# Kernel optimization log

Hardware: AMD Instinct MI355X
Metric: run time of the kernel (lower is better)

Reference implementation:

```python
import jax, jax.numpy as jnp
import numpy as np


def setup_inputs() -> dict:
    key = jax.random.key(0)
    ks = jax.random.split(key, 5)
    N, D, H, E = 8192, 1024, 4096, 8
    s = 0.02
    return {
        "x": jax.random.normal(ks[0], (N, D), jnp.float32),
        "Wr": jax.random.normal(ks[1], (D, E), jnp.float32) * s,
        "br": jnp.zeros((E,), jnp.float32),
        "W1": jax.random.normal(ks[2], (E, D, H), jnp.float32) * s,
        "b1": jnp.zeros((E, H), jnp.float32),
        "W2": jax.random.normal(ks[3], (E, H, D), jnp.float32) * s,
        "b2": jnp.zeros((E, D), jnp.float32),
        "k": 2,
    }


def reference(x, Wr, br, W1, b1, W2, b2, k):
    # Router (eval mode: no gate noise)
    logits = x @ Wr + br                      # [N, E]
    scores = jax.nn.softmax(logits, axis=-1)  # [N, E]
    topk_vals, topk_inds = jax.lax.top_k(scores, k)  # [N, k]
    N, E = scores.shape
    # dispatch_mask: zeros scattered with top-k probabilities
    dispatch_mask = jnp.zeros_like(scores).at[
        jnp.arange(N)[:, None], topk_inds
    ].set(topk_vals)                          # [N, E]
    # Dense all-expert FFN compute (faithful to the original wasteful pattern)
    h = jax.nn.relu(jnp.einsum('nd,edh->neh', x, W1) + b1)   # [N, E, H]
    expert_outputs = jnp.einsum('neh,ehd->ned', h, W2) + b2  # [N, E, D]
    output = jnp.einsum('ned,ne->nd', expert_outputs, dispatch_mask)  # [N, D]
    # Load-balancing aux loss (torch.var is unbiased, ddof=1)
    importance = dispatch_mask.sum(axis=0)    # [E]
    imp_mean = jnp.mean(importance)
    imp_var = jnp.var(importance, ddof=1)
    aux_loss = imp_var / (imp_mean ** 2 + 1e-9)
    return output, aux_loss
```

## Files before the change

### kernel.cpp

```cpp
#include <hip/hip_runtime.h>
#include <hip/hip_bf16.h>


#define NTOK 8192
#define DDIM 1024
#define HDIM 4096
#define NEXP 8
#define NASSIGN (NTOK * 2)
#define MAX_MT 72
#define KSPLIT 4

typedef __bf16 bf16_t;
typedef __bf16 bf16x4 __attribute__((ext_vector_type(4)));
typedef __bf16 bf16x8 __attribute__((ext_vector_type(8)));
typedef float f32x4 __attribute__((ext_vector_type(4)));

#define GLOAD16(gptr, lptr)                                                    \
  __builtin_amdgcn_global_load_lds(                                            \
      (const __attribute__((address_space(1))) void*)(gptr),                   \
      (__attribute__((address_space(3))) void*)(lptr), 16, 0, 0)


__global__ void __launch_bounds__(256) transpose_cvt_kernel(
    const float* __restrict__ in, bf16_t* __restrict__ out, int R, int C) {
  __shared__ float tile[32][33];
  const size_t mat = (size_t)R * C;
  const float* ip = in + (size_t)blockIdx.z * mat;
  bf16_t* op = out + (size_t)blockIdx.z * mat;
  const int c0 = blockIdx.x * 32, r0 = blockIdx.y * 32;
  const int tx = threadIdx.x, ty = threadIdx.y;
#pragma unroll
  for (int i = 0; i < 4; ++i) {
    const int r = ty + 8 * i;
    tile[r][tx] = ip[(size_t)(r0 + r) * C + (c0 + tx)];
  }
  __syncthreads();
#pragma unroll
  for (int i = 0; i < 4; ++i) {
    const int r = ty + 8 * i;
    op[(size_t)(c0 + r) * R + (r0 + tx)] = (bf16_t)tile[tx][r];
  }
}


__global__ void __launch_bounds__(256) router_kernel(
    const float* __restrict__ x, const float* __restrict__ Wr,
    const float* __restrict__ br, int2* __restrict__ ids,
    float2* __restrict__ prs, int* __restrict__ counts,
    bf16_t* __restrict__ xb) {
  const int n = blockIdx.x;
  const int t = threadIdx.x;
  const float4 xv = ((const float4*)(x + (size_t)n * DDIM))[t];
  bf16x4 o;
  o[0] = (bf16_t)xv.x; o[1] = (bf16_t)xv.y;
  o[2] = (bf16_t)xv.z; o[3] = (bf16_t)xv.w;
  ((bf16x4*)(xb + (size_t)n * DDIM))[t] = o;

  float acc[NEXP];
#pragma unroll
  for (int e = 0; e < NEXP; ++e) acc[e] = 0.f;
  const float xq[4] = {xv.x, xv.y, xv.z, xv.w};
#pragma unroll
  for (int q = 0; q < 4; ++q) {
    const float* w = Wr + (size_t)(4 * t + q) * NEXP;
#pragma unroll
    for (int e = 0; e < NEXP; ++e) acc[e] += xq[q] * w[e];
  }
  __shared__ float red[256][NEXP];
#pragma unroll
  for (int e = 0; e < NEXP; ++e) red[t][e] = acc[e];
  __syncthreads();
  for (int s = 128; s >= 1; s >>= 1) {
    if (t < s) {
#pragma unroll
      for (int e = 0; e < NEXP; ++e) red[t][e] += red[t + s][e];
    }
    __syncthreads();
  }
  if (t == 0) {
    float l[NEXP];
#pragma unroll
    for (int e = 0; e < NEXP; ++e) l[e] = red[0][e] + br[e];
    int i1 = 0; float v1 = l[0];
    for (int e = 1; e < NEXP; ++e)
      if (l[e] > v1) { v1 = l[e]; i1 = e; }
    int i2 = (i1 == 0) ? 1 : 0; float v2 = l[i2];
    for (int e = 0; e < NEXP; ++e)
      if (e != i1 && l[e] > v2) { v2 = l[e]; i2 = e; }
    float denom = 0.f;
    for (int e = 0; e < NEXP; ++e) denom += expf(l[e] - v1);
    const float p1 = 1.f / denom;
    const float p2 = expf(v2 - v1) / denom;
    ids[n] = make_int2(i1, i2);
    prs[n] = make_float2(p1, p2);
    atomicAdd(&counts[i1], 1);
    atomicAdd(&counts[i2], 1);
  }
}

__global__ void __launch_bounds__(256) scan_aux_kernel(
    const int* __restrict__ counts, int* __restrict__ offsets,
    int* __restrict__ tmap, const int2* __restrict__ ids,
    const float2* __restrict__ prs, float* __restrict__ aux_out) {
  const int t = threadIdx.x;
  if (t == 0) {
    int off = 0, nt = 0;
    for (int e = 0; e < NEXP; ++e) {
      offsets[e] = off;
      const int c = counts[e];
      for (int m0 = 0; m0 < c; m0 += 256) {
        tmap[nt] = e;
        tmap[MAX_MT + nt] = m0;
        ++nt;
      }
      off += c;
    }
    offsets[NEXP] = off;
    tmap[2 * MAX_MT] = nt;
  }
  float imp[NEXP];
#pragma unroll
  for (int e = 0; e < NEXP; ++e) imp[e] = 0.f;
  for (int n = t; n < NTOK; n += 256) {
    const int2 id = ids[n];
    const float2 pr = prs[n];
#pragma unroll
    for (int e = 0; e < NEXP; ++e)
      imp[e] += (id.x == e ? pr.x : 0.f) + (id.y == e ? pr.y : 0.f);
  }
  __shared__ float red[256][NEXP];
#pragma unroll
  for (int e = 0; e < NEXP; ++e) red[t][e] = imp[e];
  __syncthreads();
  for (int s = 128; s >= 1; s >>= 1) {
    if (t < s) {
#pragma unroll
      for (int e = 0; e < NEXP; ++e) red[t][e] += red[t + s][e];
    }
    __syncthreads();
  }
  if (t == 0) {
    float m = 0.f;
    for (int e = 0; e < NEXP; ++e) m += red[0][e];
    m *= (1.f / NEXP);
    float v = 0.f;
    for (int e = 0; e < NEXP; ++e) {
      const float d = red[0][e] - m;
      v += d * d;
    }
    v *= (1.f / (NEXP - 1));
    aux_out[0] = v / (m * m + 1e-9f);
  }
}

__global__ void __launch_bounds__(256) scatter_kernel(
    const int2* __restrict__ ids, const float2* __restrict__ prs,
    const int* __restrict__ offsets, int* __restrict__ cursor,
    int* __restrict__ btok, float* __restrict__ bprob) {
  const int n = blockIdx.x * 256 + threadIdx.x;
  if (n >= NTOK) return;
  const int2 id = ids[n];
  const float2 pr = prs[n];
  int p = atomicAdd(&cursor[id.x], 1);
  btok[offsets[id.x] + p] = n;
  bprob[offsets[id.x] + p] = pr.x;
  p = atomicAdd(&cursor[id.y], 1);
  btok[offsets[id.y] + p] = n;
  bprob[offsets[id.y] + p] = pr.y;
}


__global__ void __launch_bounds__(512, 2) gemm1_kernel(
    const bf16_t* __restrict__ xb, const bf16_t* __restrict__ W1t,
    const float* __restrict__ b1, const int* __restrict__ btok,
    const int* __restrict__ offsets, const int* __restrict__ counts,
    const int* __restrict__ tmap, bf16_t* __restrict__ h) {
  const int tidx = blockIdx.y;
  if (tidx >= tmap[2 * MAX_MT]) return;
  const int e = tmap[tidx];
  const int m0 = tmap[MAX_MT + tidx];
  const int cnt = counts[e];
  const int aoff = offsets[e];
  const int n0 = blockIdx.x * 256;

  __shared__ __align__(16) bf16_t Al[2][256 * 64];
  __shared__ __align__(16) bf16_t Bl[2][256 * 64];

  const int tid = threadIdx.x;
  const int wave = tid >> 6;
  const int lane = tid & 63;

  const bf16_t* asrc[4];
  const bf16_t* bsrc[4];
#pragma unroll
  for (int j = 0; j < 4; ++j) {
    const int c = j * 512 + tid;
    const int r = c >> 3;
    const int kc = (c & 7) * 8;
    int arow = m0 + r;
    if (arow > cnt - 1) arow = cnt - 1;
    asrc[j] = xb + (size_t)btok[aoff + arow] * DDIM + kc;
    bsrc[j] = W1t + ((size_t)e * HDIM + n0 + r) * DDIM + kc;
  }

  f32x4 acc[8][4];
#pragma unroll
  for (int mf = 0; mf < 8; ++mf)
#pragma unroll
    for (int nf = 0; nf < 4; ++nf) acc[mf][nf] = (f32x4){0.f, 0.f, 0.f, 0.f};

  const int wr = (wave >> 2) * 128;
  const int wc = (wave & 3) * 64;
  const int lrow = lane & 15;
  const int lk8 = (lane >> 4) * 8;

  auto stage = [&](int b, int t) {
    const int ko = t * 64;
    char* Ab = (char*)&Al[b][0] + wave * 1024;
    char* Bb = (char*)&Bl[b][0] + wave * 1024;
#pragma unroll
    for (int j = 0; j < 4; ++j) {
      GLOAD16(asrc[j] + ko, Ab + j * 8192);
      GLOAD16(bsrc[j] + ko, Bb + j * 8192);
    }
  };
  auto compute = [&](int b) {
    const bf16_t* Ab = &Al[b][0];
    const bf16_t* Bb = &Bl[b][0];
    __builtin_amdgcn_s_setprio(1);
#pragma unroll
    for (int ks = 0; ks < 2; ++ks) {
      bf16x8 af[8], bfr[4];
#pragma unroll
      for (int mf = 0; mf < 8; ++mf)
        af[mf] = *(const bf16x8*)&Ab[(wr + mf * 16 + lrow) * 64 + ks * 32 + lk8];
#pragma unroll
      for (int nf = 0; nf < 4; ++nf)
        bfr[nf] = *(const bf16x8*)&Bb[(wc + nf * 16 + lrow) * 64 + ks * 32 + lk8];
#pragma unroll
      for (int mf = 0; mf < 8; ++mf)
#pragma unroll
        for (int nf = 0; nf < 4; ++nf)
          acc[mf][nf] = __builtin_amdgcn_mfma_f32_16x16x32_bf16(
              af[mf], bfr[nf], acc[mf][nf], 0, 0, 0);
    }
    __builtin_amdgcn_s_setprio(0);
  };

  stage(0, 0);
  __syncthreads();
#pragma unroll
  for (int t = 0; t < 16; t += 2) {
    stage(1, t + 1);
    compute(0);
    __syncthreads();
    if (t + 2 < 16) stage(0, t + 2);
    compute(1);
    __syncthreads();
  }

  const int rbase = (lane >> 4) * 4;
  const float* b1e = b1 + (size_t)e * HDIM + n0;
#pragma unroll
  for (int nf = 0; nf < 4; ++nf) {
    const int cl = wc + nf * 16 + lrow;
    const float bb = b1e[cl];
#pragma unroll
    for (int mf = 0; mf < 8; ++mf) {
#pragma unroll
      for (int r = 0; r < 4; ++r) {
        const int grow = wr + mf * 16 + rbase + r;
        if (m0 + grow < cnt)
          h[(size_t)(aoff + m0 + grow) * HDIM + (n0 + cl)] =
              (bf16_t)fmaxf(acc[mf][nf][r] + bb, 0.f);
      }
    }
  }
}

__global__ void __launch_bounds__(512, 2) gemm2_kernel(
    const bf16_t* __restrict__ h, const bf16_t* __restrict__ W2t,
    const float* __restrict__ b2, const int* __restrict__ btok,
    const float* __restrict__ bprob, const int* __restrict__ offsets,
    const int* __restrict__ counts, const int* __restrict__ tmap,
    float* __restrict__ out) {
  const int tidx = blockIdx.y >> 2;
  const int kch = blockIdx.y & 3;
  if (tidx >= tmap[2 * MAX_MT]) return;
  const int e = tmap[tidx];
  const int m0 = tmap[MAX_MT + tidx];
  const int cnt = counts[e];
  const int aoff = offsets[e];
  const int n0 = blockIdx.x * 256;

  __shared__ __align__(16) bf16_t Al[2][256 * 64];
  __shared__ __align__(16) bf16_t Bl[2][256 * 64];

  const int tid = threadIdx.x;
  const int wave = tid >> 6;
  const int lane = tid & 63;

  const bf16_t* asrc[4];
  const bf16_t* bsrc[4];
#pragma unroll
  for (int j = 0; j < 4; ++j) {
    const int c = j * 512 + tid;
    const int r = c >> 3;
    const int kc = (c & 7) * 8 + kch * 1024;
    int arow = m0 + r;
    if (arow > cnt - 1) arow = cnt - 1;
    asrc[j] = h + (size_t)(aoff + arow) * HDIM + kc;
    bsrc[j] = W2t + ((size_t)e * DDIM + n0 + r) * HDIM + kc;
  }

  f32x4 acc[8][4];
#pragma unroll
  for (int mf = 0; mf < 8; ++mf)
#pragma unroll
    for (int nf = 0; nf < 4; ++nf) acc[mf][nf] = (f32x4){0.f, 0.f, 0.f, 0.f};

  const int wr = (wave >> 2) * 128;
  const int wc = (wave & 3) * 64;
  const int lrow = lane & 15;
  const int lk8 = (lane >> 4) * 8;

  auto stage = [&](int b, int t) {
    const int ko = t * 64;
    char* Ab = (char*)&Al[b][0] + wave * 1024;
    char* Bb = (char*)&Bl[b][0] + wave * 1024;
#pragma unroll
    for (int j = 0; j < 4; ++j) {
      GLOAD16(asrc[j] + ko, Ab + j * 8192);
      GLOAD16(bsrc[j] + ko, Bb + j * 8192);
    }
  };
  auto compute = [&](int b) {
    const bf16_t* Ab = &Al[b][0];
    const bf16_t* Bb = &Bl[b][0];
    __builtin_amdgcn_s_setprio(1);
#pragma unroll
    for (int ks = 0; ks < 2; ++ks) {
      bf16x8 af[8], bfr[4];
#pragma unroll
      for (int mf = 0; mf < 8; ++mf)
        af[mf] = *(const bf16x8*)&Ab[(wr + mf * 16 + lrow) * 64 + ks * 32 + lk8];
#pragma unroll
      for (int nf = 0; nf < 4; ++nf)
        bfr[nf] = *(const bf16x8*)&Bb[(wc + nf * 16 + lrow) * 64 + ks * 32 + lk8];
#pragma unroll
      for (int mf = 0; mf < 8; ++mf)
#pragma unroll
        for (int nf = 0; nf < 4; ++nf)
          acc[mf][nf] = __builtin_amdgcn_mfma_f32_16x16x32_bf16(
              af[mf], bfr[nf], acc[mf][nf], 0, 0, 0);
    }
    __builtin_amdgcn_s_setprio(0);
  };

  stage(0, 0);
  __syncthreads();
#pragma unroll
  for (int t = 0; t < 16; t += 2) {
    stage(1, t + 1);
    compute(0);
    __syncthreads();
    if (t + 2 < 16) stage(0, t + 2);
    compute(1);
    __syncthreads();
  }

  const int rbase = (lane >> 4) * 4;
  const float* b2e = b2 + (size_t)e * DDIM + n0;
  float bb[4];
#pragma unroll
  for (int nf = 0; nf < 4; ++nf)
    bb[nf] = (kch == 0) ? b2e[wc + nf * 16 + lrow] : 0.f;
#pragma unroll
  for (int mf = 0; mf < 8; ++mf) {
#pragma unroll
    for (int r = 0; r < 4; ++r) {
      const int grow = wr + mf * 16 + rbase + r;
      if (m0 + grow < cnt) {
        const int assign = aoff + m0 + grow;
        const int tok = btok[assign];
        const float p = bprob[assign];
        float* orow = out + (size_t)tok * DDIM + n0;
#pragma unroll
        for (int nf = 0; nf < 4; ++nf) {
          const int cl = wc + nf * 16 + lrow;
          atomicAdd(&orow[cl], (acc[mf][nf][r] + bb[nf]) * p);
        }
      }
    }
  }
}


extern "C" void kernel_launch(void* const* d_in, const int* in_sizes, int n_in,
                              void* d_out, int out_size, void* d_ws,
                              size_t ws_size, hipStream_t stream) {
  const float* x = (const float*)d_in[0];
  const float* Wr = (const float*)d_in[1];
  const float* br = (const float*)d_in[2];
  const float* W1 = (const float*)d_in[3];
  const float* b1 = (const float*)d_in[4];
  const float* W2 = (const float*)d_in[5];
  const float* b2 = (const float*)d_in[6];

  char* w = (char*)d_ws;
  auto alloc = [&](size_t bytes) -> char* {
    char* p = w;
    w += (bytes + 255) & ~(size_t)255;
    return p;
  };
  bf16_t* xb = (bf16_t*)alloc((size_t)NTOK * DDIM * 2);
  bf16_t* W1t = (bf16_t*)alloc((size_t)NEXP * DDIM * HDIM * 2);
  bf16_t* W2t = (bf16_t*)alloc((size_t)NEXP * DDIM * HDIM * 2);
  bf16_t* hbuf = (bf16_t*)alloc((size_t)NASSIGN * HDIM * 2);
  int* btok = (int*)alloc(NASSIGN * 4);
  float* bprob = (float*)alloc(NASSIGN * 4);
  int2* ids = (int2*)alloc(NTOK * 8);
  float2* prs = (float2*)alloc(NTOK * 8);
  int* ctrl = (int*)alloc(64);
  int* offsets = (int*)alloc(64);
  int* tmap = (int*)alloc((2 * MAX_MT + 1) * 4);
  int* counts = ctrl;
  int* cursor = ctrl + 8;
  (void)in_sizes; (void)n_in; (void)ws_size;

  float* out = (float*)d_out;

  hipMemsetAsync(d_out, 0, (size_t)out_size * 4, stream);
  hipMemsetAsync(ctrl, 0, 64, stream);

  transpose_cvt_kernel<<<dim3(HDIM / 32, DDIM / 32, NEXP), dim3(32, 8), 0,
                         stream>>>(W1, W1t, DDIM, HDIM);
  transpose_cvt_kernel<<<dim3(DDIM / 32, HDIM / 32, NEXP), dim3(32, 8), 0,
                         stream>>>(W2, W2t, HDIM, DDIM);
  router_kernel<<<NTOK, 256, 0, stream>>>(x, Wr, br, ids, prs, counts, xb);
  scan_aux_kernel<<<1, 256, 0, stream>>>(counts, offsets, tmap, ids, prs,
                                         out + (size_t)NTOK * DDIM);
  scatter_kernel<<<NTOK / 256, 256, 0, stream>>>(ids, prs, offsets, cursor,
                                                 btok, bprob);
  gemm1_kernel<<<dim3(HDIM / 256, MAX_MT, 1), 512, 0, stream>>>(
      xb, W1t, b1, btok, offsets, counts, tmap, hbuf);
  gemm2_kernel<<<dim3(DDIM / 256, MAX_MT * KSPLIT, 1), 512, 0, stream>>>(
      hbuf, W2t, b2, btok, bprob, offsets, counts, tmap, out);
}
```

Baseline: 1.015 ms.

## Retile expert GEMMs to 128x128 triple-buffered, swizzled LDS with XCD remap

Both grouped GEMMs move from 256x256 tiles with 512 threads and double buffering to 128x128x32 tiles with 256 threads, triple-buffered global_load_lds staging, explicit vmcnt waits and raw barriers. LDS slots are XOR-swizzled to avoid bank conflicts, and blocks are remapped across XCDs for cache locality. The router reduction now uses wave shuffles, and the weight transpose writes packed bf16 pairs from 64-row tiles. Smaller tiles give more blocks and better occupancy, at the cost of lower per-block operand reuse and more atomic epilogue traffic.

After: 941.3 us. 7.2% less time.

```diff
diff --git a/kernel.cpp b/kernel.cpp
--- a/kernel.cpp
+++ b/kernel.cpp
@@ -7,10 +7,12 @@
 #define HDIM 4096
 #define NEXP 8
 #define NASSIGN (NTOK * 2)
-#define MAX_MT 72
-#define KSPLIT 4
+#define MAX_MT 135
+#define GRID1 (32 * MAX_MT)
+#define GRID2 (8 * 4 * MAX_MT)
 
 typedef __bf16 bf16_t;
+typedef __bf16 bf16x2 __attribute__((ext_vector_type(2)));
 typedef __bf16 bf16x4 __attribute__((ext_vector_type(4)));
 typedef __bf16 bf16x8 __attribute__((ext_vector_type(8)));
 typedef float f32x4 __attribute__((ext_vector_type(4)));
@@ -20,28 +22,36 @@
       (const __attribute__((address_space(1))) void*)(gptr),                   \
       (__attribute__((address_space(3))) void*)(lptr), 16, 0, 0)
 
+#define VMCNT(n) asm volatile("s_waitcnt vmcnt(" #n ")" ::: "memory")
+
+__device__ __forceinline__ int xcd_swz(int orig, int nwg) {
+  const int cpx = nwg >> 3;
+  return (orig & 7) * cpx + (orig >> 3);
+}
 
 __global__ void __launch_bounds__(256) transpose_cvt_kernel(
     const float* __restrict__ in, bf16_t* __restrict__ out, int R, int C) {
-  __shared__ float tile[32][33];
+  __shared__ float tile[64][33];
   const size_t mat = (size_t)R * C;
   const float* ip = in + (size_t)blockIdx.z * mat;
   bf16_t* op = out + (size_t)blockIdx.z * mat;
-  const int c0 = blockIdx.x * 32, r0 = blockIdx.y * 32;
+  const int c0 = blockIdx.x * 32, r0 = blockIdx.y * 64;
   const int tx = threadIdx.x, ty = threadIdx.y;
 #pragma unroll
-  for (int i = 0; i < 4; ++i) {
+  for (int i = 0; i < 8; ++i) {
     const int r = ty + 8 * i;
     tile[r][tx] = ip[(size_t)(r0 + r) * C + (c0 + tx)];
   }
   __syncthreads();
 #pragma unroll
-  for (int i = 0; i < 4; ++i) {
-    const int r = ty + 8 * i;
-    op[(size_t)(c0 + r) * R + (r0 + tx)] = (bf16_t)tile[tx][r];
-  }
-}
-
+  for (int j = 0; j < 4; ++j) {
+    const int c = ty + 8 * j;
+    bf16x2 v;
+    v[0] = (bf16_t)tile[2 * tx][c];
+    v[1] = (bf16_t)tile[2 * tx + 1][c];
+    *(bf16x2*)(op + (size_t)(c0 + c) * R + r0 + 2 * tx) = v;
+  }
+}
 
 __global__ void __launch_bounds__(256) router_kernel(
     const float* __restrict__ x, const float* __restrict__ Wr,
@@ -50,6 +60,7 @@
     bf16_t* __restrict__ xb) {
   const int n = blockIdx.x;
   const int t = threadIdx.x;
+  const int wave = t >> 6, lane = t & 63;
   const float4 xv = ((const float4*)(x + (size_t)n * DDIM))[t];
   bf16x4 o;
   o[0] = (bf16_t)xv.x; o[1] = (bf16_t)xv.y;
@@ -66,21 +77,20 @@
 #pragma unroll
     for (int e = 0; e < NEXP; ++e) acc[e] += xq[q] * w[e];
   }
-  __shared__ float red[256][NEXP];
-#pragma unroll
-  for (int e = 0; e < NEXP; ++e) red[t][e] = acc[e];
+#pragma unroll
+  for (int off = 32; off >= 1; off >>= 1)
+#pragma unroll
+    for (int e = 0; e < NEXP; ++e) acc[e] += __shfl_down(acc[e], off);
+  __shared__ float red[4][NEXP];
+  if (lane == 0)
+#pragma unroll
+    for (int e = 0; e < NEXP; ++e) red[wave][e] = acc[e];
   __syncthreads();
-  for (int s = 128; s >= 1; s >>= 1) {
-    if (t < s) {
-#pragma unroll
-      for (int e = 0; e < NEXP; ++e) red[t][e] += red[t + s][e];
-    }
-    __syncthreads();
-  }
   if (t == 0) {
     float l[NEXP];
 #pragma unroll
-    for (int e = 0; e < NEXP; ++e) l[e] = red[0][e] + br[e];
+    for (int e = 0; e < NEXP; ++e)
+      l[e] = ((red[0][e] + red[1][e]) + (red[2][e] + red[3][e])) + br[e];
     int i1 = 0; float v1 = l[0];
     for (int e = 1; e < NEXP; ++e)
       if (l[e] > v1) { v1 = l[e]; i1 = e; }
@@ -89,10 +99,8 @@
       if (e != i1 && l[e] > v2) { v2 = l[e]; i2 = e; }
     float denom = 0.f;
     for (int e = 0; e < NEXP; ++e) denom += expf(l[e] - v1);
-    const float p1 = 1.f / denom;
-    const float p2 = expf(v2 - v1) / denom;
     ids[n] = make_int2(i1, i2);
-    prs[n] = make_float2(p1, p2);
+    prs[n] = make_float2(1.f / denom, expf(v2 - v1) / denom);
     atomicAdd(&counts[i1], 1);
     atomicAdd(&counts[i2], 1);
   }
@@ -108,7 +116,7 @@
     for (int e = 0; e < NEXP; ++e) {
       offsets[e] = off;
       const int c = counts[e];
-      for (int m0 = 0; m0 < c; m0 += 256) {
+      for (int m0 = 0; m0 < c; m0 += 128) {
         tmap[nt] = e;
         tmap[MAX_MT + nt] = m0;
         ++nt;
@@ -170,94 +178,106 @@
 }
 
 
-__global__ void __launch_bounds__(512, 2) gemm1_kernel(
+__global__ void __launch_bounds__(256, 3) gemm1_kernel(
     const bf16_t* __restrict__ xb, const bf16_t* __restrict__ W1t,
     const float* __restrict__ b1, const int* __restrict__ btok,
     const int* __restrict__ offsets, const int* __restrict__ counts,
     const int* __restrict__ tmap, bf16_t* __restrict__ h) {
-  const int tidx = blockIdx.y;
+  const int job = xcd_swz((int)blockIdx.x, GRID1);
+  const int tidx = job >> 5;
+  const int nblk = job & 31;
   if (tidx >= tmap[2 * MAX_MT]) return;
   const int e = tmap[tidx];
   const int m0 = tmap[MAX_MT + tidx];
   const int cnt = counts[e];
   const int aoff = offsets[e];
-  const int n0 = blockIdx.x * 256;
-
-  __shared__ __align__(16) bf16_t Al[2][256 * 64];
-  __shared__ __align__(16) bf16_t Bl[2][256 * 64];
+  const int n0 = nblk * 128;
+
+  __shared__ __align__(16) bf16_t Al[3][128 * 32];
+  __shared__ __align__(16) bf16_t Bl[3][128 * 32];
 
   const int tid = threadIdx.x;
   const int wave = tid >> 6;
   const int lane = tid & 63;
 
-  const bf16_t* asrc[4];
-  const bf16_t* bsrc[4];
-#pragma unroll
-  for (int j = 0; j < 4; ++j) {
-    const int c = j * 512 + tid;
-    const int r = c >> 3;
-    const int kc = (c & 7) * 8;
+  const bf16_t* asrc[2];
+  const bf16_t* bsrc[2];
+#pragma unroll
+  for (int j = 0; j < 2; ++j) {
+    const int c = j * 256 + tid;
+    const int r = c >> 2;
+    const int slot = (c & 3) ^ ((r >> 1) & 3);
     int arow = m0 + r;
     if (arow > cnt - 1) arow = cnt - 1;
-    asrc[j] = xb + (size_t)btok[aoff + arow] * DDIM + kc;
-    bsrc[j] = W1t + ((size_t)e * HDIM + n0 + r) * DDIM + kc;
-  }
-
-  f32x4 acc[8][4];
-#pragma unroll
-  for (int mf = 0; mf < 8; ++mf)
+    asrc[j] = xb + (size_t)btok[aoff + arow] * DDIM + slot * 8;
+    bsrc[j] = W1t + ((size_t)e * HDIM + n0 + r) * DDIM + slot * 8;
+  }
+
+  const int wr = (wave >> 1) * 64;
+  const int wc = (wave & 1) * 64;
+  const int lrow = lane & 15;
+  const int lslot = lane >> 4;
+
+  int aoffb[4], boffb[4];
+#pragma unroll
+  for (int f = 0; f < 4; ++f) {
+    const int Rr = wr + f * 16 + lrow;
+    aoffb[f] = Rr * 64 + ((lslot ^ ((Rr >> 1) & 3)) << 4);
+    const int Cc = wc + f * 16 + lrow;
+    boffb[f] = Cc * 64 + ((lslot ^ ((Cc >> 1) & 3)) << 4);
+  }
+
+  f32x4 acc[4][4];
+#pragma unroll
+  for (int mf = 0; mf < 4; ++mf)
 #pragma unroll
     for (int nf = 0; nf < 4; ++nf) acc[mf][nf] = (f32x4){0.f, 0.f, 0.f, 0.f};
 
-  const int wr = (wave >> 2) * 128;
-  const int wc = (wave & 3) * 64;
-  const int lrow = lane & 15;
-  const int lk8 = (lane >> 4) * 8;
-
   auto stage = [&](int b, int t) {
-    const int ko = t * 64;
     char* Ab = (char*)&Al[b][0] + wave * 1024;
     char* Bb = (char*)&Bl[b][0] + wave * 1024;
-#pragma unroll
-    for (int j = 0; j < 4; ++j) {
-      GLOAD16(asrc[j] + ko, Ab + j * 8192);
-      GLOAD16(bsrc[j] + ko, Bb + j * 8192);
+    const int ko = t * 32;
+#pragma unroll
+    for (int j = 0; j < 2; ++j) {
+      GLOAD16(asrc[j] + ko, Ab + j * 4096);
+      GLOAD16(bsrc[j] + ko, Bb + j * 4096);
     }
   };
   auto compute = [&](int b) {
-    const bf16_t* Ab = &Al[b][0];
-    const bf16_t* Bb = &Bl[b][0];
+    const char* Ab = (const char*)&Al[b][0];
+    const char* Bb = (const char*)&Bl[b][0];
+    bf16x8 af[4], bfr[4];
+#pragma unroll
+    for (int f = 0; f < 4; ++f) {
+      af[f] = *(const bf16x8*)(Ab + aoffb[f]);
+      bfr[f] = *(const bf16x8*)(Bb + boffb[f]);
+    }
     __builtin_amdgcn_s_setprio(1);
 #pragma unroll
-    for (int ks = 0; ks < 2; ++ks) {
-      bf16x8 af[8], bfr[4];
-#pragma unroll
-      for (int mf = 0; mf < 8; ++mf)
-        af[mf] = *(const bf16x8*)&Ab[(wr + mf * 16 + lrow) * 64 + ks * 32 + lk8];
+    for (int mf = 0; mf < 4; ++mf)
 #pragma unroll
       for (int nf = 0; nf < 4; ++nf)
-        bfr[nf] = *(const bf16x8*)&Bb[(wc + nf * 16 + lrow) * 64 + ks * 32 + lk8];
-#pragma unroll
-      for (int mf = 0; mf < 8; ++mf)
-#pragma unroll
-        for (int nf = 0; nf < 4; ++nf)
-          acc[mf][nf] = __builtin_amdgcn_mfma_f32_16x16x32_bf16(
-              af[mf], bfr[nf], acc[mf][nf], 0, 0, 0);
-    }
+        acc[mf][nf] = __builtin_amdgcn_mfma_f32_16x16x32_bf16(
+            af[mf], bfr[nf], acc[mf][nf], 0, 0, 0);
     __builtin_amdgcn_s_setprio(0);
   };
 
   stage(0, 0);
-  __syncthreads();
-#pragma unroll
-  for (int t = 0; t < 16; t += 2) {
-    stage(1, t + 1);
-    compute(0);
-    __syncthreads();
-    if (t + 2 < 16) stage(0, t + 2);
-    compute(1);
-    __syncthreads();
-  }
+  stage(1, 1);
+  int cb = 0, pb = 2;
+  for (int t = 0; t < 31; ++t) {
+    VMCNT(4);
+    __builtin_amdgcn_s_barrier();
+    __builtin_amdgcn_sched_barrier(0);
+    if (t + 2 < 32) stage(pb, t + 2);
+    compute(cb);
+    cb = (cb == 2) ? 0 : cb + 1;
+    pb = (pb == 2) ? 0 : pb + 1;
+  }
+  VMCNT(0);
+  __builtin_amdgcn_s_barrier();
+  __builtin_amdgcn_sched_barrier(0);
+  compute(cb);
 
   const int rbase = (lane >> 4) * 4;
   const float* b1e = b1 + (size_t)e * HDIM + n0;
@@ -266,7 +286,7 @@
     const int cl = wc + nf * 16 + lrow;
     const float bb = b1e[cl];
 #pragma unroll
-    for (int mf = 0; mf < 8; ++mf) {
+    for (int mf = 0; mf < 4; ++mf) {
 #pragma unroll
       for (int r = 0; r < 4; ++r) {
         const int grow = wr + mf * 16 + rbase + r;
@@ -278,96 +298,108 @@
   }
 }
 
-__global__ void __launch_bounds__(512, 2) gemm2_kernel(
+__global__ void __launch_bounds__(256, 3) gemm2_kernel(
     const bf16_t* __restrict__ h, const bf16_t* __restrict__ W2t,
     const float* __restrict__ b2, const int* __restrict__ btok,
     const float* __restrict__ bprob, const int* __restrict__ offsets,
     const int* __restrict__ counts, const int* __restrict__ tmap,
     float* __restrict__ out) {
-  const int tidx = blockIdx.y >> 2;
-  const int kch = blockIdx.y & 3;
+  const int job = xcd_swz((int)blockIdx.x, GRID2);
+  const int tidx = job >> 5;
+  const int nblk = job & 7;
+  const int kch = (job >> 3) & 3;
   if (tidx >= tmap[2 * MAX_MT]) return;
   const int e = tmap[tidx];
   const int m0 = tmap[MAX_MT + tidx];
   const int cnt = counts[e];
   const int aoff = offsets[e];
-  const int n0 = blockIdx.x * 256;
-
-  __shared__ __align__(16) bf16_t Al[2][256 * 64];
-  __shared__ __align__(16) bf16_t Bl[2][256 * 64];
+  const int n0 = nblk * 128;
+
+  __shared__ __align__(16) bf16_t Al[3][128 * 32];
+  __shared__ __align__(16) bf16_t Bl[3][128 * 32];
 
   const int tid = threadIdx.x;
   const int wave = tid >> 6;
   const int lane = tid & 63;
 
-  const bf16_t* asrc[4];
-  const bf16_t* bsrc[4];
-#pragma unroll
-  for (int j = 0; j < 4; ++j) {
-    const int c = j * 512 + tid;
-    const int r = c >> 3;
-    const int kc = (c & 7) * 8 + kch * 1024;
+  const bf16_t* asrc[2];
+  const bf16_t* bsrc[2];
+#pragma unroll
+  for (int j = 0; j < 2; ++j) {
+    const int c = j * 256 + tid;
+    const int r = c >> 2;
+    const int slot = (c & 3) ^ ((r >> 1) & 3);
     int arow = m0 + r;
     if (arow > cnt - 1) arow = cnt - 1;
-    asrc[j] = h + (size_t)(aoff + arow) * HDIM + kc;
-    bsrc[j] = W2t + ((size_t)e * DDIM + n0 + r) * HDIM + kc;
-  }
-
-  f32x4 acc[8][4];
-#pragma unroll
-  for (int mf = 0; mf < 8; ++mf)
+    asrc[j] = h + (size_t)(aoff + arow) * HDIM + kch * 1024 + slot * 8;
+    bsrc[j] = W2t + ((size_t)e * DDIM + n0 + r) * HDIM + kch * 1024 + slot * 8;
+  }
+
+  const int wr = (wave >> 1) * 64;
+  const int wc = (wave & 1) * 64;
+  const int lrow = lane & 15;
+  const int lslot = lane >> 4;
+
+  int aoffb[4], boffb[4];
+#pragma unroll
+  for (int f = 0; f < 4; ++f) {
+    const int Rr = wr + f * 16 + lrow;
+    aoffb[f] = Rr * 64 + ((lslot ^ ((Rr >> 1) & 3)) << 4);
+    const int Cc = wc + f * 16 + lrow;
+    boffb[f] = Cc * 64 + ((lslot ^ ((Cc >> 1) & 3)) << 4);
+  }
+
+  f32x4 acc[4][4];
+#pragma unroll
+  for (int mf = 0; mf < 4; ++mf)
 #pragma unroll
     for (int nf = 0; nf < 4; ++nf) acc[mf][nf] = (f32x4){0.f, 0.f, 0.f, 0.f};
 
-  const int wr = (wave >> 2) * 128;
-  const int wc = (wave & 3) * 64;
-  const int lrow = lane & 15;
-  const int lk8 = (lane >> 4) * 8;
-
   auto stage = [&](int b, int t) {
-    const int ko = t * 64;
     char* Ab = (char*)&Al[b][0] + wave * 1024;
     char* Bb = (char*)&Bl[b][0] + wave * 1024;
-#pragma unroll
-    for (int j = 0; j < 4; ++j) {
-      GLOAD16(asrc[j] + ko, Ab + j * 8192);
-      GLOAD16(bsrc[j] + ko, Bb + j * 8192);
+    const int ko = t * 32;
+#pragma unroll
+    for (int j = 0; j < 2; ++j) {
+      GLOAD16(asrc[j] + ko, Ab + j * 4096);
+      GLOAD16(bsrc[j] + ko, Bb + j * 4096);
     }
   };
   auto compute = [&](int b) {
-    const bf16_t* Ab = &Al[b][0];
-    const bf16_t* Bb = &Bl[b][0];
+    const char* Ab = (const char*)&Al[b][0];
+    const char* Bb = (const char*)&Bl[b][0];
+    bf16x8 af[4], bfr[4];
+#pragma unroll
+    for (int f = 0; f < 4; ++f) {
+      af[f] = *(const bf16x8*)(Ab + aoffb[f]);
+      bfr[f] = *(const bf16x8*)(Bb + boffb[f]);
+    }
     __builtin_amdgcn_s_setprio(1);
 #pragma unroll
-    for (int ks = 0; ks < 2; ++ks) {
-      bf16x8 af[8], bfr[4];
-#pragma unroll
-      for (int mf = 0; mf < 8; ++mf)
-        af[mf] = *(const bf16x8*)&Ab[(wr + mf * 16 + lrow) * 64 + ks * 32 + lk8];
+    for (int mf = 0; mf < 4; ++mf)
 #pragma unroll
       for (int nf = 0; nf < 4; ++nf)
-        bfr[nf] = *(const bf16x8*)&Bb[(wc + nf * 16 + lrow) * 64 + ks * 32 + lk8];
-#pragma unroll
-      for (int mf = 0; mf < 8; ++mf)
-#pragma unroll
-        for (int nf = 0; nf < 4; ++nf)
-          acc[mf][nf] = __builtin_amdgcn_mfma_f32_16x16x32_bf16(
-              af[mf], bfr[nf], acc[mf][nf], 0, 0, 0);
-    }
+        acc[mf][nf] = __builtin_amdgcn_mfma_f32_16x16x32_bf16(
+            af[mf], bfr[nf], acc[mf][nf], 0, 0, 0);
     __builtin_amdgcn_s_setprio(0);
   };
 
   stage(0, 0);
-  __syncthreads();
-#pragma unroll
-  for (int t = 0; t < 16; t += 2) {
-    stage(1, t + 1);
-    compute(0);
-    __syncthreads();
-    if (t + 2 < 16) stage(0, t + 2);
-    compute(1);
-    __syncthreads();
-  }
+  stage(1, 1);
+  int cb = 0, pb = 2;
+  for (int t = 0; t < 31; ++t) {
+    VMCNT(4);
+    __builtin_amdgcn_s_barrier();
+    __builtin_amdgcn_sched_barrier(0);
+    if (t + 2 < 32) stage(pb, t + 2);
+    compute(cb);
+    cb = (cb == 2) ? 0 : cb + 1;
+    pb = (pb == 2) ? 0 : pb + 1;
+  }
+  VMCNT(0);
+  __builtin_amdgcn_s_barrier();
+  __builtin_amdgcn_sched_barrier(0);
+  compute(cb);
 
   const int rbase = (lane >> 4) * 4;
   const float* b2e = b2 + (size_t)e * DDIM + n0;
@@ -376,7 +408,7 @@
   for (int nf = 0; nf < 4; ++nf)
     bb[nf] = (kch == 0) ? b2e[wc + nf * 16 + lrow] : 0.f;
 #pragma unroll
-  for (int mf = 0; mf < 8; ++mf) {
+  for (int mf = 0; mf < 4; ++mf) {
 #pragma unroll
     for (int r = 0; r < 4; ++r) {
       const int grow = wr + mf * 16 + rbase + r;
@@ -433,17 +465,17 @@
   hipMemsetAsync(d_out, 0, (size_t)out_size * 4, stream);
   hipMemsetAsync(ctrl, 0, 64, stream);
 
-  transpose_cvt_kernel<<<dim3(HDIM / 32, DDIM / 32, NEXP), dim3(32, 8), 0,
+  transpose_cvt_kernel<<<dim3(HDIM / 32, DDIM / 64, NEXP), dim3(32, 8), 0,
                          stream>>>(W1, W1t, DDIM, HDIM);
-  transpose_cvt_kernel<<<dim3(DDIM / 32, HDIM / 32, NEXP), dim3(32, 8), 0,
+  transpose_cvt_kernel<<<dim3(DDIM / 32, HDIM / 64, NEXP), dim3(32, 8), 0,
                          stream>>>(W2, W2t, HDIM, DDIM);
   router_kernel<<<NTOK, 256, 0, stream>>>(x, Wr, br, ids, prs, counts, xb);
   scan_aux_kernel<<<1, 256, 0, stream>>>(counts, offsets, tmap, ids, prs,
                                          out + (size_t)NTOK * DDIM);
   scatter_kernel<<<NTOK / 256, 256, 0, stream>>>(ids, prs, offsets, cursor,
                                                  btok, bprob);
-  gemm1_kernel<<<dim3(HDIM / 256, MAX_MT, 1), 512, 0, stream>>>(
-      xb, W1t, b1, btok, offsets, counts, tmap, hbuf);
-  gemm2_kernel<<<dim3(DDIM / 256, MAX_MT * KSPLIT, 1), 512, 0, stream>>>(
-      hbuf, W2t, b2, btok, bprob, offsets, counts, tmap, out);
-}
+  gemm1_kernel<<<GRID1, 256, 0, stream>>>(xb, W1t, b1, btok, offsets, counts,
+                                          tmap, hbuf);
+  gemm2_kernel<<<GRID2, 256, 0, stream>>>(hbuf, W2t, b2, btok, bprob, offsets,
+                                          counts, tmap, out);
+}
```
